# Kernel tuning notes

Hardware: AMD Instinct MI355X
Metric: run time of the kernel (lower is better)

The kernel has to match this reference:

```python
import jax, jax.numpy as jnp
import numpy as np

B, IN, H = 4096, 2048, 2048
STD = 1.0 / np.sqrt(H)


def setup_inputs() -> dict:
    key = jax.random.key(0)
    ks = jax.random.split(key, 16)
    uni = lambda k, shape: jax.random.uniform(k, shape, jnp.float32, -STD, STD)
    inp = {
        "x": jax.random.normal(ks[0], (B, IN), jnp.float32),
        "h": jax.random.normal(ks[1], (B, H), jnp.float32),
        "c": jax.random.normal(ks[2], (B, H), jnp.float32),
        # weights are used untransposed via th.mm(x, w): w_x* must be [IN, H]-compatible,
        # which in the original requires IN == H; shapes kept as [H, IN].
        "w_xi": uni(ks[3], (H, IN)), "w_xf": uni(ks[4], (H, IN)),
        "w_xo": uni(ks[5], (H, IN)), "w_xc": uni(ks[6], (H, IN)),
        "w_hi": uni(ks[7], (H, H)), "w_hf": uni(ks[8], (H, H)),
        "w_ho": uni(ks[9], (H, H)), "w_hc": uni(ks[10], (H, H)),
        "b_i": uni(ks[11], (H,)), "b_f": uni(ks[12], (H,)),
        "b_o": uni(ks[13], (H,)), "b_c": uni(ks[14], (H,)),
    }
    return inp


def reference(x, h, c, w_xi, w_xf, w_xo, w_xc, w_hi, w_hf, w_ho, w_hc,
              b_i, b_f, b_o, b_c):
    # Fused form of the 8 small GEMMs: concat gate weights along output dim.
    Wx = jnp.concatenate([w_xi, w_xf, w_xo, w_xc], axis=1)  # [IN, 4H]
    Wh = jnp.concatenate([w_hi, w_hf, w_ho, w_hc], axis=1)  # [H, 4H]
    b = jnp.concatenate([b_i, b_f, b_o, b_c])               # [4H]
    gates = x @ Wx + h @ Wh + b                              # [B, 4H]
    i_t, f_t, o_t, g_t = jnp.split(gates, 4, axis=1)
    i_t = jax.nn.sigmoid(i_t)
    f_t = jax.nn.sigmoid(f_t)
    o_t = jax.nn.sigmoid(o_t)
    g_t = jnp.tanh(g_t)
    c_t = c * f_t + i_t * g_t
    h_t = o_t * jnp.tanh(c_t)
    # original reshapes to [B, 1, H]
    return h_t[:, None, :], c_t[:, None, :]
```

## Files before the change

kernel.cpp:

```cpp
#include <hip/hip_runtime.h>
#include <stdint.h>

typedef unsigned short u16;
typedef __bf16 bf16x8 __attribute__((ext_vector_type(8)));
typedef float f32x4 __attribute__((ext_vector_type(4)));
typedef unsigned short u16x8 __attribute__((ext_vector_type(8)));
typedef unsigned short u16x4 __attribute__((ext_vector_type(4)));

#define B_ROWS 4096
#define H_DIM  2048
#define K_DIM  4096
#define N_DIM  8192

__device__ __forceinline__ u16 f2b(float f) {
  union { float f; unsigned int i; } v; v.f = f;
  unsigned int i = v.i;
  return (u16)((i + 0x7fffu + ((i >> 16) & 1u)) >> 16);
}
__device__ __forceinline__ float b2f(u16 u) {
  union { unsigned int i; float f; } v; v.i = ((unsigned int)u) << 16; return v.f;
}
__device__ __forceinline__ float sigmoidf_(float x) { return 1.0f / (1.0f + __expf(-x)); }
__device__ __forceinline__ float tanhf_(float x)    { return 1.0f - 2.0f / (__expf(2.0f * x) + 1.0f); }

__device__ __forceinline__ void glds16(const u16* g, u16* l) {
  __builtin_amdgcn_global_load_lds(
      (__attribute__((address_space(1))) void*)(g),
      (__attribute__((address_space(3))) void*)(l), 16, 0, 0);
}

struct WPtrs { const float* p[8]; };

__global__ __launch_bounds__(256) void convert_A(const float* __restrict__ X,
                                                 const float* __restrict__ Hs,
                                                 u16* __restrict__ Abf) {
  const int idx = blockIdx.x * 256 + threadIdx.x;
  const int b = idx >> 9;
  const int c = (idx & 511) * 8;
  const float* src = (c < H_DIM) ? (X + (size_t)b * H_DIM + c)
                                 : (Hs + (size_t)b * H_DIM + (c - H_DIM));
  float4 v0 = *(const float4*)(src);
  float4 v1 = *(const float4*)(src + 4);
  u16x8 o;
  o[0] = f2b(v0.x); o[1] = f2b(v0.y); o[2] = f2b(v0.z); o[3] = f2b(v0.w);
  o[4] = f2b(v1.x); o[5] = f2b(v1.y); o[6] = f2b(v1.z); o[7] = f2b(v1.w);
  *(u16x8*)(Abf + (size_t)b * K_DIM + c) = o;
}

__global__ __launch_bounds__(256) void transpose_w(WPtrs wp, u16* __restrict__ Wt) {
  __shared__ __align__(16) u16 tile[64][72];
  const int jt = blockIdx.x;
  const int kt = blockIdx.y;
  const int z  = blockIdx.z;
  const int s = z >> 2, g = z & 3;
  const float* __restrict__ w = wp.p[z];
  const int tid = threadIdx.x;
  const int j0 = jt * 64, k0 = kt * 64;

  const int c4 = (tid & 15) * 4;
  const int r0 = tid >> 4;
#pragma unroll
  for (int it = 0; it < 4; ++it) {
    int r = r0 + it * 16;
    float4 v = *(const float4*)(w + (size_t)(k0 + r) * H_DIM + j0 + c4);
    tile[r][c4 + 0] = f2b(v.x);
    tile[r][c4 + 1] = f2b(v.y);
    tile[r][c4 + 2] = f2b(v.z);
    tile[r][c4 + 3] = f2b(v.w);
  }
  __syncthreads();

  const int cc = (tid & 7) * 8;
  const int jr0 = tid >> 3;
#pragma unroll
  for (int it = 0; it < 2; ++it) {
    int jr = jr0 + it * 32;
    u16x8 v;
#pragma unroll
    for (int i = 0; i < 8; ++i) v[i] = tile[cc + i][jr];
    size_t orow = (size_t)(g * H_DIM + j0 + jr);
    *(u16x8*)(Wt + orow * K_DIM + (size_t)(s * H_DIM + k0 + cc)) = v;
  }
}

__global__ __launch_bounds__(256) void gemm_gates(const u16* __restrict__ A,
                                                  const u16* __restrict__ Wt,
                                                  u16* __restrict__ gates) {
  __shared__ __align__(16) u16 sA[128 * 32];
  __shared__ __align__(16) u16 sB[128 * 32];
  const int tid = threadIdx.x;
  const int wave = tid >> 6, lane = tid & 63;
  const int bm = blockIdx.x & 31;
  const int bn = blockIdx.x >> 5;
  const int wr = (wave >> 1) * 64;
  const int wc = (wave & 1) * 64;

  const int c0 = wave * 2;
  const int row0 = c0 * 16 + (lane >> 2);
  const int row1 = row0 + 16;
  const int kc0 = (lane & 3) ^ ((row0 >> 1) & 3);
  const int kc1 = (lane & 3) ^ ((row1 >> 1) & 3);
  const size_t gA0 = (size_t)(bm * 128 + row0) * K_DIM + kc0 * 8;
  const size_t gA1 = (size_t)(bm * 128 + row1) * K_DIM + kc1 * 8;
  const size_t gB0 = (size_t)(bn * 128 + row0) * K_DIM + kc0 * 8;
  const size_t gB1 = (size_t)(bn * 128 + row1) * K_DIM + kc1 * 8;
  u16* ldsA0 = sA + c0 * 512;
  u16* ldsA1 = sA + (c0 + 1) * 512;
  u16* ldsB0 = sB + c0 * 512;
  u16* ldsB1 = sB + (c0 + 1) * 512;

  const int q = lane >> 4;
  int aOff[4], bOff[4];
#pragma unroll
  for (int i = 0; i < 4; ++i) {
    int ra = wr + i * 16 + (lane & 15);
    aOff[i] = ra * 32 + ((q ^ ((ra >> 1) & 3)) * 8);
    int rb = wc + i * 16 + (lane & 15);
    bOff[i] = rb * 32 + ((q ^ ((rb >> 1) & 3)) * 8);
  }

  f32x4 acc[4][4] = {};

  for (int kt = 0; kt < K_DIM / 32; ++kt) {
    const int kg = kt * 32;
    __syncthreads();
    glds16(A + gA0 + kg, ldsA0);
    glds16(A + gA1 + kg, ldsA1);
    glds16(Wt + gB0 + kg, ldsB0);
    glds16(Wt + gB1 + kg, ldsB1);
    __syncthreads();

    bf16x8 af[4], bf[4];
#pragma unroll
    for (int i = 0; i < 4; ++i) af[i] = *reinterpret_cast<const bf16x8*>(sA + aOff[i]);
#pragma unroll
    for (int i = 0; i < 4; ++i) bf[i] = *reinterpret_cast<const bf16x8*>(sB + bOff[i]);
#pragma unroll
    for (int mi = 0; mi < 4; ++mi)
#pragma unroll
      for (int ni = 0; ni < 4; ++ni)
        acc[mi][ni] = __builtin_amdgcn_mfma_f32_16x16x32_bf16(af[mi], bf[ni], acc[mi][ni], 0, 0, 0);
  }

  const int rbase = bm * 128 + wr + (lane >> 4) * 4;
  const int cbase = bn * 128 + wc + (lane & 15);
#pragma unroll
  for (int mi = 0; mi < 4; ++mi) {
#pragma unroll
    for (int ni = 0; ni < 4; ++ni) {
      size_t base = (size_t)(rbase + mi * 16) * N_DIM + (size_t)(cbase + ni * 16);
#pragma unroll
      for (int r = 0; r < 4; ++r)
        gates[base + (size_t)r * N_DIM] = f2b(acc[mi][ni][r]);
    }
  }
}

__global__ __launch_bounds__(256) void lstm_epilogue(
    const u16* __restrict__ gates, const float* __restrict__ Cin,
    const float* __restrict__ Bi, const float* __restrict__ Bf,
    const float* __restrict__ Bo, const float* __restrict__ Bc,
    float* __restrict__ Out) {
  const int idx = blockIdx.x * 256 + threadIdx.x;
  const int b = idx >> 9;
  const int j = (idx & 511) * 4;
  const size_t gbase = (size_t)b * N_DIM + j;
  u16x4 iv = *(const u16x4*)(gates + gbase);
  u16x4 fv = *(const u16x4*)(gates + gbase + 2048);
  u16x4 ov = *(const u16x4*)(gates + gbase + 4096);
  u16x4 gv = *(const u16x4*)(gates + gbase + 6144);
  float4 cv  = *(const float4*)(Cin + (size_t)b * H_DIM + j);
  float4 biv = *(const float4*)(Bi + j);
  float4 bfv = *(const float4*)(Bf + j);
  float4 bov = *(const float4*)(Bo + j);
  float4 bcv = *(const float4*)(Bc + j);
  float ce[4] = {cv.x, cv.y, cv.z, cv.w};
  float bie[4] = {biv.x, biv.y, biv.z, biv.w};
  float bfe[4] = {bfv.x, bfv.y, bfv.z, bfv.w};
  float boe[4] = {bov.x, bov.y, bov.z, bov.w};
  float bce[4] = {bcv.x, bcv.y, bcv.z, bcv.w};
  float4 hv, ctv;
  float he[4], cte[4];
#pragma unroll
  for (int e = 0; e < 4; ++e) {
    float it = sigmoidf_(b2f(iv[e]) + bie[e]);
    float ft = sigmoidf_(b2f(fv[e]) + bfe[e]);
    float ot = sigmoidf_(b2f(ov[e]) + boe[e]);
    float gt = tanhf_(b2f(gv[e]) + bce[e]);
    float ct = ce[e] * ft + it * gt;
    he[e] = ot * tanhf_(ct);
    cte[e] = ct;
  }
  hv.x = he[0]; hv.y = he[1]; hv.z = he[2]; hv.w = he[3];
  ctv.x = cte[0]; ctv.y = cte[1]; ctv.z = cte[2]; ctv.w = cte[3];
  *(float4*)(Out + (size_t)b * H_DIM + j) = hv;
  *(float4*)(Out + (size_t)B_ROWS * H_DIM + (size_t)b * H_DIM + j) = ctv;
}

extern "C" void kernel_launch(void* const* d_in, const int* in_sizes, int n_in,
                              void* d_out, int out_size, void* d_ws, size_t ws_size,
                              hipStream_t stream) {
  const float* X   = (const float*)d_in[0];
  const float* Hs  = (const float*)d_in[1];
  const float* Cin = (const float*)d_in[2];
  WPtrs wp;
  for (int i = 0; i < 8; ++i) wp.p[i] = (const float*)d_in[3 + i];
  const float* Bi = (const float*)d_in[11];
  const float* Bf = (const float*)d_in[12];
  const float* Bo = (const float*)d_in[13];
  const float* Bc = (const float*)d_in[14];

  u16* Wt    = (u16*)d_ws;
  u16* Abf   = Wt + (size_t)N_DIM * K_DIM;
  u16* gates = Abf + (size_t)B_ROWS * K_DIM;
  float* Out = (float*)d_out;

  convert_A<<<(B_ROWS * K_DIM / 8) / 256, 256, 0, stream>>>(X, Hs, Abf);
  transpose_w<<<dim3(32, 32, 8), 256, 0, stream>>>(wp, Wt);
  gemm_gates<<<32 * 64, 256, 0, stream>>>(Abf, Wt, gates);
  lstm_epilogue<<<(B_ROWS * H_DIM / 4) / 256, 256, 0, stream>>>(gates, Cin, Bi, Bf, Bo, Bc, Out);
}
```

Baseline: 590.7 us.

## Fuse LSTM epilogue into GEMM via gate-interleaved weight layout

Reorders the transposed weight rows so the four gates of each hidden unit sit next to each other, letting each GEMM output tile hold complete i/f/o/g groups. The LSTM cell math then runs inside the GEMM epilogue after staging accumulators through shared memory, with biases interleaved by a small prep kernel. This removes the bf16 gates round-trip through global memory and a separate launch, at the cost of extra LDS syncs and staging in the GEMM tail. The transpose tile padding is also changed.

Result: slower. 638.2 us (+8.0%).

```diff
diff --git a/kernel.cpp b/kernel.cpp
--- a/kernel.cpp
+++ b/kernel.cpp
@@ -5,7 +5,6 @@
 typedef __bf16 bf16x8 __attribute__((ext_vector_type(8)));
 typedef float f32x4 __attribute__((ext_vector_type(4)));
 typedef unsigned short u16x8 __attribute__((ext_vector_type(8)));
-typedef unsigned short u16x4 __attribute__((ext_vector_type(4)));
 
 #define B_ROWS 4096
 #define H_DIM  2048
@@ -17,9 +16,6 @@
   unsigned int i = v.i;
   return (u16)((i + 0x7fffu + ((i >> 16) & 1u)) >> 16);
 }
-__device__ __forceinline__ float b2f(u16 u) {
-  union { unsigned int i; float f; } v; v.i = ((unsigned int)u) << 16; return v.f;
-}
 __device__ __forceinline__ float sigmoidf_(float x) { return 1.0f / (1.0f + __expf(-x)); }
 __device__ __forceinline__ float tanhf_(float x)    { return 1.0f - 2.0f / (__expf(2.0f * x) + 1.0f); }
 
@@ -30,6 +26,17 @@
 }
 
 struct WPtrs { const float* p[8]; };
+
+__global__ __launch_bounds__(256) void prep_bias(const float* __restrict__ Bi,
+                                                 const float* __restrict__ Bf,
+                                                 const float* __restrict__ Bo,
+                                                 const float* __restrict__ Bc,
+                                                 float* __restrict__ biasI) {
+  const int j = blockIdx.x * 256 + threadIdx.x;
+  float4 v;
+  v.x = Bi[j]; v.y = Bf[j]; v.z = Bo[j]; v.w = Bc[j];
+  *(float4*)(biasI + (size_t)j * 4) = v;
+}
 
 __global__ __launch_bounds__(256) void convert_A(const float* __restrict__ X,
                                                  const float* __restrict__ Hs,
@@ -48,7 +55,7 @@
 }
 
 __global__ __launch_bounds__(256) void transpose_w(WPtrs wp, u16* __restrict__ Wt) {
-  __shared__ __align__(16) u16 tile[64][72];
+  __shared__ u16 tile[64][70];
   const int jt = blockIdx.x;
   const int kt = blockIdx.y;
   const int z  = blockIdx.z;
@@ -78,16 +85,21 @@
     u16x8 v;
 #pragma unroll
     for (int i = 0; i < 8; ++i) v[i] = tile[cc + i][jr];
-    size_t orow = (size_t)(g * H_DIM + j0 + jr);
+    size_t orow = (size_t)(4 * (j0 + jr) + g);
     *(u16x8*)(Wt + orow * K_DIM + (size_t)(s * H_DIM + k0 + cc)) = v;
   }
 }
 
-__global__ __launch_bounds__(256) void gemm_gates(const u16* __restrict__ A,
-                                                  const u16* __restrict__ Wt,
-                                                  u16* __restrict__ gates) {
-  __shared__ __align__(16) u16 sA[128 * 32];
-  __shared__ __align__(16) u16 sB[128 * 32];
+__global__ __launch_bounds__(256) void gemm_lstm(const u16* __restrict__ A,
+                                                 const u16* __restrict__ Wt,
+                                                 const float* __restrict__ biasI,
+                                                 const float* __restrict__ Cin,
+                                                 float* __restrict__ Out) {
+  __shared__ __align__(16) unsigned char smem[132 * 32 * 4];
+  u16* sA = (u16*)smem;
+  u16* sB = (u16*)(smem + 8192);
+  float* L = (float*)smem;
+
   const int tid = threadIdx.x;
   const int wave = tid >> 6, lane = tid & 63;
   const int bm = blockIdx.x & 31;
@@ -142,59 +154,45 @@
         acc[mi][ni] = __builtin_amdgcn_mfma_f32_16x16x32_bf16(af[mi], bf[ni], acc[mi][ni], 0, 0, 0);
   }
 
-  const int rbase = bm * 128 + wr + (lane >> 4) * 4;
-  const int cbase = bn * 128 + wc + (lane & 15);
+  const int slotb = (wave >> 1) * 16 + (lane >> 4) * 4;
+  const int rslot = tid >> 3;
+  const int j0l   = (tid & 7) * 4;
+  const int jg    = bn * 32 + j0l;
+  const size_t cbase = (size_t)B_ROWS * H_DIM;
+
 #pragma unroll
   for (int mi = 0; mi < 4; ++mi) {
+    __syncthreads();
 #pragma unroll
     for (int ni = 0; ni < 4; ++ni) {
-      size_t base = (size_t)(rbase + mi * 16) * N_DIM + (size_t)(cbase + ni * 16);
+      int colb = wc + ni * 16 + (lane & 15);
 #pragma unroll
       for (int r = 0; r < 4; ++r)
-        gates[base + (size_t)r * N_DIM] = f2b(acc[mi][ni][r]);
+        L[(size_t)(slotb + r) * 132 + colb] = acc[mi][ni][r];
     }
-  }
-}
-
-__global__ __launch_bounds__(256) void lstm_epilogue(
-    const u16* __restrict__ gates, const float* __restrict__ Cin,
-    const float* __restrict__ Bi, const float* __restrict__ Bf,
-    const float* __restrict__ Bo, const float* __restrict__ Bc,
-    float* __restrict__ Out) {
-  const int idx = blockIdx.x * 256 + threadIdx.x;
-  const int b = idx >> 9;
-  const int j = (idx & 511) * 4;
-  const size_t gbase = (size_t)b * N_DIM + j;
-  u16x4 iv = *(const u16x4*)(gates + gbase);
-  u16x4 fv = *(const u16x4*)(gates + gbase + 2048);
-  u16x4 ov = *(const u16x4*)(gates + gbase + 4096);
-  u16x4 gv = *(const u16x4*)(gates + gbase + 6144);
-  float4 cv  = *(const float4*)(Cin + (size_t)b * H_DIM + j);
-  float4 biv = *(const float4*)(Bi + j);
-  float4 bfv = *(const float4*)(Bf + j);
-  float4 bov = *(const float4*)(Bo + j);
-  float4 bcv = *(const float4*)(Bc + j);
-  float ce[4] = {cv.x, cv.y, cv.z, cv.w};
-  float bie[4] = {biv.x, biv.y, biv.z, biv.w};
-  float bfe[4] = {bfv.x, bfv.y, bfv.z, bfv.w};
-  float boe[4] = {bov.x, bov.y, bov.z, bov.w};
-  float bce[4] = {bcv.x, bcv.y, bcv.z, bcv.w};
-  float4 hv, ctv;
-  float he[4], cte[4];
-#pragma unroll
-  for (int e = 0; e < 4; ++e) {
-    float it = sigmoidf_(b2f(iv[e]) + bie[e]);
-    float ft = sigmoidf_(b2f(fv[e]) + bfe[e]);
-    float ot = sigmoidf_(b2f(ov[e]) + boe[e]);
-    float gt = tanhf_(b2f(gv[e]) + bce[e]);
-    float ct = ce[e] * ft + it * gt;
-    he[e] = ot * tanhf_(ct);
-    cte[e] = ct;
-  }
-  hv.x = he[0]; hv.y = he[1]; hv.z = he[2]; hv.w = he[3];
-  ctv.x = cte[0]; ctv.y = cte[1]; ctv.z = cte[2]; ctv.w = cte[3];
-  *(float4*)(Out + (size_t)b * H_DIM + j) = hv;
-  *(float4*)(Out + (size_t)B_ROWS * H_DIM + (size_t)b * H_DIM + j) = ctv;
+    __syncthreads();
+
+    const int row_glob = bm * 128 + (rslot >> 4) * 64 + mi * 16 + (rslot & 15);
+    float4 cin4 = *(const float4*)(Cin + (size_t)row_glob * H_DIM + jg);
+    float ce[4] = {cin4.x, cin4.y, cin4.z, cin4.w};
+    float he[4], cte[4];
+#pragma unroll
+    for (int e = 0; e < 4; ++e) {
+      float4 g4 = *(const float4*)&L[(size_t)rslot * 132 + (j0l + e) * 4];
+      float4 b4 = *(const float4*)(biasI + (size_t)(jg + e) * 4);
+      float it = sigmoidf_(g4.x + b4.x);
+      float ft = sigmoidf_(g4.y + b4.y);
+      float ot = sigmoidf_(g4.z + b4.z);
+      float gt = tanhf_(g4.w + b4.w);
+      float ct = ce[e] * ft + it * gt;
+      he[e]  = ot * tanhf_(ct);
+      cte[e] = ct;
+    }
+    float4 hv;  hv.x = he[0];  hv.y = he[1];  hv.z = he[2];  hv.w = he[3];
+    float4 cv;  cv.x = cte[0]; cv.y = cte[1]; cv.z = cte[2]; cv.w = cte[3];
+    *(float4*)(Out + (size_t)row_glob * H_DIM + jg) = hv;
+    *(float4*)(Out + cbase + (size_t)row_glob * H_DIM + jg) = cv;
+  }
 }
 
 extern "C" void kernel_launch(void* const* d_in, const int* in_sizes, int n_in,
@@ -210,13 +208,13 @@
   const float* Bo = (const float*)d_in[13];
   const float* Bc = (const float*)d_in[14];
 
-  u16* Wt    = (u16*)d_ws;
-  u16* Abf   = Wt + (size_t)N_DIM * K_DIM;
-  u16* gates = Abf + (size_t)B_ROWS * K_DIM;
-  float* Out = (float*)d_out;
-
+  u16* Wt      = (u16*)d_ws;
+  u16* Abf     = Wt + (size_t)N_DIM * K_DIM;
+  float* biasI = (float*)(Abf + (size_t)B_ROWS * K_DIM);
+  float* Out   = (float*)d_out;
+
+  prep_bias<<<H_DIM / 256, 256, 0, stream>>>(Bi, Bf, Bo, Bc, biasI);
   convert_A<<<(B_ROWS * K_DIM / 8) / 256, 256, 0, stream>>>(X, Hs, Abf);
   transpose_w<<<dim3(32, 32, 8), 256, 0, stream>>>(wp, Wt);
-  gemm_gates<<<32 * 64, 256, 0, stream>>>(Abf, Wt, gates);
-  lstm_epilogue<<<(B_ROWS * H_DIM / 4) / 256, 256, 0, stream>>>(gates, Cin, Bi, Bf, Bo, Bc, Out);
-}
+  gemm_lstm<<<32 * 64, 256, 0, stream>>>(Abf, Wt, biasI, Cin, Out);
+}
```
